# Optimization experiments

Measured on AMD Instinct MI355X. Metric: run time of the kernel, lower is better.

Reference implementation:

```python
import jax, jax.numpy as jnp
import numpy as np

N_NODES = 50000
N_EDGES = 800000
D_IN = 128
D_HID = 128
N_CLS = 47


def setup_inputs() -> dict:
    key = jax.random.key(0)
    ks = jax.random.split(key, 10)
    inp = {
        "features": jax.random.normal(ks[0], (N_NODES, D_IN), dtype=jnp.float32),
        "src": jax.random.randint(ks[1], (N_EDGES,), 0, N_NODES),
        "dst": jax.random.randint(ks[2], (N_EDGES,), 0, N_NODES),
        "Wself0": jax.random.normal(ks[3], (D_IN, D_HID), dtype=jnp.float32) / np.sqrt(D_IN),
        "Wneigh0": jax.random.normal(ks[4], (D_IN, D_HID), dtype=jnp.float32) / np.sqrt(D_IN),
        "b0": jnp.zeros((D_HID,), dtype=jnp.float32),
        "Wself1": jax.random.normal(ks[5], (D_HID, D_HID), dtype=jnp.float32) / np.sqrt(D_HID),
        "Wneigh1": jax.random.normal(ks[6], (D_HID, D_HID), dtype=jnp.float32) / np.sqrt(D_HID),
        "b1": jnp.zeros((D_HID,), dtype=jnp.float32),
        "Wself2": jax.random.normal(ks[7], (D_HID, N_CLS), dtype=jnp.float32) / np.sqrt(D_HID),
        "Wneigh2": jax.random.normal(ks[8], (D_HID, N_CLS), dtype=jnp.float32) / np.sqrt(D_HID),
        "b2": jnp.zeros((N_CLS,), dtype=jnp.float32),
    }
    return inp


def reference(features, src, dst, Wself0, Wneigh0, b0, Wself1, Wneigh1, b1, Wself2, Wneigh2, b2):
    # GraphSAGE (DGL SAGEConv, aggregator_type='mean', eval mode so dropout is identity).
    # Per layer: h_neigh[v] = mean_{(u->v) in E} h[u]; out = h @ W_self + h_neigh @ W_neigh + b
    n = features.shape[0]
    # in-degree for mean aggregation (zero-degree nodes get zero neighbor feature)
    deg = jax.ops.segment_sum(jnp.ones(dst.shape, dtype=features.dtype), dst, num_segments=n)
    inv_deg = (1.0 / jnp.maximum(deg, 1.0))[:, None]  # [N,1]

    def sage_layer(h, Ws, Wn, b, act):
        # gather src features per edge, scatter-add into dst, normalize by in-degree
        agg = jax.ops.segment_sum(h[src], dst, num_segments=n) * inv_deg  # [N, d]
        out = h @ Ws + agg @ Wn + b
        return jax.nn.relu(out) if act else out

    h = sage_layer(features, Wself0, Wneigh0, b0, True)
    h = sage_layer(h, Wself1, Wneigh1, b1, True)
    h = sage_layer(h, Wself2, Wneigh2, b2, False)
    return h
```

## Files before the change

kernel.cpp:

```cpp
#include <hip/hip_runtime.h>

#define D 128
#define NCLS 47
#define CAP 64

typedef short short8 __attribute__((ext_vector_type(8)));
typedef float floatx4 __attribute__((ext_vector_type(4)));
typedef unsigned short ushort8 __attribute__((ext_vector_type(8)));

__device__ inline float bf16lo(unsigned int u) {
    union { unsigned int i; float f; } c; c.i = u << 16; return c.f;
}
__device__ inline float bf16hi(unsigned int u) {
    union { unsigned int i; float f; } c; c.i = u & 0xffff0000u; return c.f;
}
__device__ inline unsigned short f2bf(float f) {
    union { float f; unsigned int i; } c; c.f = f;
    unsigned int r = c.i + 0x7fffu + ((c.i >> 16) & 1u);
    return (unsigned short)(r >> 16);
}
__device__ inline unsigned int pack2(float x, float y) {
    return (unsigned int)f2bf(x) | ((unsigned int)f2bf(y) << 16);
}

__global__ void zero_cnt_kernel(int* __restrict__ cnt, int n) {
    int i = blockIdx.x * blockDim.x + threadIdx.x;
    if (i < n) cnt[i] = 0;
}

#define FB 1024
#define PB 1024
__global__ __launch_bounds__(256) void fill_prep_kernel(
    const int* __restrict__ src, const int* __restrict__ dst,
    int* __restrict__ cnt, unsigned short* __restrict__ csr, int n_edges,
    const float* __restrict__ f, unsigned int* __restrict__ hA,
    unsigned int* __restrict__ hB, int npairs, int n,
    const float* __restrict__ Ws0, const float* __restrict__ Wn0, unsigned short* __restrict__ Wt0,
    const float* __restrict__ Ws1, const float* __restrict__ Wn1, unsigned short* __restrict__ Wt1,
    const float* __restrict__ Ws2, const float* __restrict__ Wn2, unsigned short* __restrict__ Wt2) {
    if (blockIdx.x < FB) {
        int cohort = blockIdx.x & 7;
        int cb = blockIdx.x >> 3;
        int nth = (FB >> 3) * 256;
        int tid = cb * 256 + threadIdx.x;
        int range = (n + 7) >> 3;
        int lo = cohort * range;
        int hi = lo + range;
        if (hi > n) hi = n;
        for (int e = tid; e < n_edges; e += nth) {
            int d = dst[e];
            if (d >= lo && d < hi) {
                int pos = atomicAdd(&cnt[d], 1);
                if (pos < CAP) csr[d * CAP + pos] = (unsigned short)src[e];
            }
        }
        return;
    }
    int tid = (blockIdx.x - FB) * 256 + threadIdx.x;
    int total = npairs + 128  + 2 * 128 * 256 + 48 * 256;
    for (int gid = tid; gid < total; gid += PB * 256) {
        if (gid < npairs) {
            float2 v = ((const float2*)f)[gid];
            hA[gid] = pack2(v.x, v.y);
            continue;
        }
        int r = gid - npairs;
        if (r < 128) {
            if (r < 64) hA[(size_t)n * 64 + r] = 0u;
            else hB[(size_t)n * 64 + (r - 64)] = 0u;
            continue;
        }
        r -= 128;
        if (r < 128 * 256) {
            int nn = r >> 8, k = r & 255;
            float v = (k < 128) ? Ws0[k * 128 + nn] : Wn0[(k - 128) * 128 + nn];
            Wt0[nn * 256 + k] = f2bf(v);
            continue;
        }
        r -= 128 * 256;
        if (r < 128 * 256) {
            int nn = r >> 8, k = r & 255;
            float v = (k < 128) ? Ws1[k * 128 + nn] : Wn1[(k - 128) * 128 + nn];
            Wt1[nn * 256 + k] = f2bf(v);
            continue;
        }
        r -= 128 * 256;
        if (r < 48 * 256) {
            int nn = r >> 8, k = r & 255;
            float v = 0.0f;
            if (nn < NCLS) v = (k < 128) ? Ws2[k * NCLS + nn] : Wn2[(k - 128) * NCLS + nn];
            Wt2[nn * 256 + k] = f2bf(v);
        }
    }
}

__global__ __launch_bounds__(256) void gather_kernel(
    const unsigned int* __restrict__ hin,
    const unsigned short* __restrict__ csr,
    const int* __restrict__ cnt,
    unsigned int* __restrict__ agg,
    int n) {
    int tid = blockIdx.x * blockDim.x + threadIdx.x;
    int node = tid >> 6;
    int lane = tid & 63;
    if (node >= n) return;
    int d = cnt[node];
    if (d > CAP) d = CAP;
    const unsigned short* crow = csr + node * CAP;
    float a0x = 0.f, a0y = 0.f, a1x = 0.f, a1y = 0.f;
    float a2x = 0.f, a2y = 0.f, a3x = 0.f, a3y = 0.f;
    int e = 0;
    for (; e + 8 <= d; e += 8) {
        ushort8 s = *(const ushort8*)(crow + e);
        unsigned int u0 = hin[(size_t)s[0] * 64 + lane];
        unsigned int u1 = hin[(size_t)s[1] * 64 + lane];
        unsigned int u2 = hin[(size_t)s[2] * 64 + lane];
        unsigned int u3 = hin[(size_t)s[3] * 64 + lane];
        unsigned int u4 = hin[(size_t)s[4] * 64 + lane];
        unsigned int u5 = hin[(size_t)s[5] * 64 + lane];
        unsigned int u6 = hin[(size_t)s[6] * 64 + lane];
        unsigned int u7 = hin[(size_t)s[7] * 64 + lane];
        a0x += bf16lo(u0); a0y += bf16hi(u0);
        a1x += bf16lo(u1); a1y += bf16hi(u1);
        a2x += bf16lo(u2); a2y += bf16hi(u2);
        a3x += bf16lo(u3); a3y += bf16hi(u3);
        a0x += bf16lo(u4); a0y += bf16hi(u4);
        a1x += bf16lo(u5); a1y += bf16hi(u5);
        a2x += bf16lo(u6); a2y += bf16hi(u6);
        a3x += bf16lo(u7); a3y += bf16hi(u7);
    }
    for (; e < d; ++e) {
        unsigned int u0 = hin[(size_t)crow[e] * 64 + lane];
        a0x += bf16lo(u0); a0y += bf16hi(u0);
    }
    float inv = 1.0f / fmaxf((float)d, 1.0f);
    float rx = ((a0x + a1x) + (a2x + a3x)) * inv;
    float ry = ((a0y + a1y) + (a2y + a3y)) * inv;
    agg[(size_t)node * 64 + lane] = pack2(rx, ry);
}

__global__ __launch_bounds__(256) void mfma_layer_kernel(
    const unsigned int* __restrict__ hin,
    const unsigned int* __restrict__ agg,
    const unsigned short* __restrict__ Wt,
    const float* __restrict__ bias,
    unsigned short* __restrict__ hout,
    int n) {
    int wave = threadIdx.x >> 6;
    int lane = threadIdx.x & 63;
    int node_base = blockIdx.x * 64 + wave * 16;
    int m = lane & 15;
    int quad = lane >> 4;
    int row_node = node_base + m;
    if (row_node >= n) row_node = n - 1;
    const unsigned short* arow = (const unsigned short*)hin + (size_t)row_node * 128;
    const unsigned short* grow = (const unsigned short*)agg + (size_t)row_node * 128;

    floatx4 acc[8];
#pragma unroll
    for (int t = 0; t < 8; ++t) acc[t] = (floatx4){0.f, 0.f, 0.f, 0.f};

#pragma unroll
    for (int ko = 0; ko < 128; ko += 32) {
        short8 a = *(const short8*)(arow + ko + quad * 8);
#pragma unroll
        for (int t = 0; t < 8; ++t) {
            short8 bfr = *(const short8*)(Wt + (size_t)(t * 16 + m) * 256 + ko + quad * 8);
            acc[t] = __builtin_amdgcn_mfma_f32_16x16x32_bf16(a, bfr, acc[t], 0, 0, 0);
        }
    }
#pragma unroll
    for (int ko = 0; ko < 128; ko += 32) {
        short8 a = *(const short8*)(grow + ko + quad * 8);
#pragma unroll
        for (int t = 0; t < 8; ++t) {
            short8 bfr = *(const short8*)(Wt + (size_t)(t * 16 + m) * 256 + 128 + ko + quad * 8);
            acc[t] = __builtin_amdgcn_mfma_f32_16x16x32_bf16(a, bfr, acc[t], 0, 0, 0);
        }
    }

#pragma unroll
    for (int t = 0; t < 8; ++t) {
        int nfeat = t * 16 + m;
        float bb = bias[nfeat];
#pragma unroll
        for (int r = 0; r < 4; ++r) {
            int node = node_base + quad * 4 + r;
            if (node < n) {
                float v = fmaxf(acc[t][r] + bb, 0.0f);
                hout[(size_t)node * 128 + nfeat] = f2bf(v);
            }
        }
    }
}

__global__ __launch_bounds__(256) void mfma_out_kernel(
    const unsigned int* __restrict__ hin,
    const unsigned int* __restrict__ agg,
    const unsigned short* __restrict__ Wt,
    const float* __restrict__ bias,
    float* __restrict__ out, int n) {
    int wave = threadIdx.x >> 6;
    int lane = threadIdx.x & 63;
    int node_base = blockIdx.x * 64 + wave * 16;
    int m = lane & 15;
    int quad = lane >> 4;
    int row_node = node_base + m;
    if (row_node >= n) row_node = n - 1;
    const unsigned short* arow = (const unsigned short*)hin + (size_t)row_node * 128;
    const unsigned short* grow = (const unsigned short*)agg + (size_t)row_node * 128;

    floatx4 acc[3];
#pragma unroll
    for (int t = 0; t < 3; ++t) acc[t] = (floatx4){0.f, 0.f, 0.f, 0.f};

#pragma unroll
    for (int ko = 0; ko < 128; ko += 32) {
        short8 a = *(const short8*)(arow + ko + quad * 8);
#pragma unroll
        for (int t = 0; t < 3; ++t) {
            short8 bfr = *(const short8*)(Wt + (size_t)(t * 16 + m) * 256 + ko + quad * 8);
            acc[t] = __builtin_amdgcn_mfma_f32_16x16x32_bf16(a, bfr, acc[t], 0, 0, 0);
        }
    }
#pragma unroll
    for (int ko = 0; ko < 128; ko += 32) {
        short8 a = *(const short8*)(grow + ko + quad * 8);
#pragma unroll
        for (int t = 0; t < 3; ++t) {
            short8 bfr = *(const short8*)(Wt + (size_t)(t * 16 + m) * 256 + 128 + ko + quad * 8);
            acc[t] = __builtin_amdgcn_mfma_f32_16x16x32_bf16(a, bfr, acc[t], 0, 0, 0);
        }
    }

#pragma unroll
    for (int t = 0; t < 3; ++t) {
        int nfeat = t * 16 + m;
        if (nfeat < NCLS) {
            float bb = bias[nfeat];
#pragma unroll
            for (int r = 0; r < 4; ++r) {
                int node = node_base + quad * 4 + r;
                if (node < n) out[(size_t)node * NCLS + nfeat] = acc[t][r] + bb;
            }
        }
    }
}

extern "C" void kernel_launch(void* const* d_in, const int* in_sizes, int n_in,
                              void* d_out, int out_size, void* d_ws, size_t ws_size,
                              hipStream_t stream) {
    const float* features = (const float*)d_in[0];
    const int* src = (const int*)d_in[1];
    const int* dst = (const int*)d_in[2];
    const float* Wself0 = (const float*)d_in[3];
    const float* Wneigh0 = (const float*)d_in[4];
    const float* b0 = (const float*)d_in[5];
    const float* Wself1 = (const float*)d_in[6];
    const float* Wneigh1 = (const float*)d_in[7];
    const float* b1 = (const float*)d_in[8];
    const float* Wself2 = (const float*)d_in[9];
    const float* Wneigh2 = (const float*)d_in[10];
    const float* b2 = (const float*)d_in[11];
    float* out = (float*)d_out;

    int n = in_sizes[0] / D;
    int n_edges = in_sizes[1];

    int* cnt = (int*)d_ws;
    unsigned short* csr = (unsigned short*)(cnt + 50048);
    unsigned int* hA = (unsigned int*)(csr + (size_t)n * CAP + 32);
    unsigned int* hB = hA + (size_t)(n + 1) * 64;
    unsigned int* agg = hB + (size_t)(n + 1) * 64;
    unsigned short* Wt0 = (unsigned short*)(agg + (size_t)n * 64);
    unsigned short* Wt1 = Wt0 + 128 * 256;
    unsigned short* Wt2 = Wt1 + 128 * 256;

    int npairs = n * 64;

    zero_cnt_kernel<<<(n + 255) / 256, 256, 0, stream>>>(cnt, n);
    fill_prep_kernel<<<FB + PB, 256, 0, stream>>>(
        src, dst, cnt, csr, n_edges,
        features, hA, hB, npairs, n,
        Wself0, Wneigh0, Wt0, Wself1, Wneigh1, Wt1, Wself2, Wneigh2, Wt2);

    int gather_blocks = (n * 64 + 255) / 256;
    int gemm_blocks = (n + 63) / 64;

    gather_kernel<<<gather_blocks, 256, 0, stream>>>(hA, csr, cnt, agg, n);
    mfma_layer_kernel<<<gemm_blocks, 256, 0, stream>>>(hA, agg, Wt0, b0, (unsigned short*)hB, n);
    gather_kernel<<<gather_blocks, 256, 0, stream>>>(hB, csr, cnt, agg, n);
    mfma_layer_kernel<<<gemm_blocks, 256, 0, stream>>>(hB, agg, Wt1, b1, (unsigned short*)hA, n);
    gather_kernel<<<gather_blocks, 256, 0, stream>>>(hA, csr, cnt, agg, n);
    mfma_out_kernel<<<gemm_blocks, 256, 0, stream>>>(hA, agg, Wt2, b2, out, n);
}
```

Measured before the change: 344.9 us.

## Fuse all stages into one persistent cooperative kernel with grid syncs

Replaces the eight separate launches (zero, fill/prep, three gathers, three GEMMs) with a single cooperative persistent kernel that separates the phases with grid-wide barriers, and keeps the multi-launch path as a fallback. Each stage becomes a grid-stride loop over nodes or tiles. The aim is to remove per-launch overhead and the idle tail between launches. In exchange the grid is capped at a fixed size, so gather and GEMM get fewer concurrent waves than the oversubscribed launches had, and each grid sync has its own cost. The zeroing of the padding rows of hA/hB is dropped, which looks harmless because the gather never reads index n.

After: 359.8 us. 1.04x slower.

```diff
diff --git a/kernel.cpp b/kernel.cpp
--- a/kernel.cpp
+++ b/kernel.cpp
@@ -1,4 +1,7 @@
 #include <hip/hip_runtime.h>
+#include <hip/hip_cooperative_groups.h>
+
+namespace cg = cooperative_groups;
 
 #define D 128
 #define NCLS 47
@@ -8,69 +11,64 @@
 typedef float floatx4 __attribute__((ext_vector_type(4)));
 typedef unsigned short ushort8 __attribute__((ext_vector_type(8)));
 
-__device__ inline float bf16lo(unsigned int u) {
+__device__ __forceinline__ float bf16lo(unsigned int u) {
     union { unsigned int i; float f; } c; c.i = u << 16; return c.f;
 }
-__device__ inline float bf16hi(unsigned int u) {
+__device__ __forceinline__ float bf16hi(unsigned int u) {
     union { unsigned int i; float f; } c; c.i = u & 0xffff0000u; return c.f;
 }
-__device__ inline unsigned short f2bf(float f) {
+__device__ __forceinline__ unsigned short f2bf(float f) {
     union { float f; unsigned int i; } c; c.f = f;
     unsigned int r = c.i + 0x7fffu + ((c.i >> 16) & 1u);
     return (unsigned short)(r >> 16);
 }
-__device__ inline unsigned int pack2(float x, float y) {
+__device__ __forceinline__ unsigned int pack2(float x, float y) {
     return (unsigned int)f2bf(x) | ((unsigned int)f2bf(y) << 16);
 }
 
-__global__ void zero_cnt_kernel(int* __restrict__ cnt, int n) {
-    int i = blockIdx.x * blockDim.x + threadIdx.x;
-    if (i < n) cnt[i] = 0;
-}
-
-#define FB 1024
-#define PB 1024
-__global__ __launch_bounds__(256) void fill_prep_kernel(
-    const int* __restrict__ src, const int* __restrict__ dst,
-    int* __restrict__ cnt, unsigned short* __restrict__ csr, int n_edges,
-    const float* __restrict__ f, unsigned int* __restrict__ hA,
-    unsigned int* __restrict__ hB, int npairs, int n,
+
+__device__ __forceinline__ void dev_zero(int* __restrict__ cnt, int n) {
+    int tid = blockIdx.x * blockDim.x + threadIdx.x;
+    int stride = gridDim.x * blockDim.x;
+    for (int i = tid; i < n; i += stride) cnt[i] = 0;
+}
+
+__device__ __forceinline__ void dev_fill(const int* __restrict__ src, const int* __restrict__ dst,
+                                         int* __restrict__ cnt, unsigned short* __restrict__ csr,
+                                         int n_edges, int n, int FBm) {
+    int cohort = blockIdx.x & 7;
+    int cb = blockIdx.x >> 3;
+    int nth = (FBm >> 3) * 256;
+    int tid = cb * 256 + threadIdx.x;
+    int range = (n + 7) >> 3;
+    int lo = cohort * range;
+    int hi = lo + range;
+    if (hi > n) hi = n;
+    for (int e = tid; e < n_edges; e += nth) {
+        int d = dst[e];
+        if (d >= lo && d < hi) {
+            int pos = atomicAdd(&cnt[d], 1);
+            if (pos < CAP) csr[d * CAP + pos] = (unsigned short)src[e];
+        }
+    }
+}
+
+__device__ __forceinline__ void dev_prep(
+    const float* __restrict__ f, unsigned int* __restrict__ hA, int npairs,
     const float* __restrict__ Ws0, const float* __restrict__ Wn0, unsigned short* __restrict__ Wt0,
     const float* __restrict__ Ws1, const float* __restrict__ Wn1, unsigned short* __restrict__ Wt1,
-    const float* __restrict__ Ws2, const float* __restrict__ Wn2, unsigned short* __restrict__ Wt2) {
-    if (blockIdx.x < FB) {
-        int cohort = blockIdx.x & 7;
-        int cb = blockIdx.x >> 3;
-        int nth = (FB >> 3) * 256;
-        int tid = cb * 256 + threadIdx.x;
-        int range = (n + 7) >> 3;
-        int lo = cohort * range;
-        int hi = lo + range;
-        if (hi > n) hi = n;
-        for (int e = tid; e < n_edges; e += nth) {
-            int d = dst[e];
-            if (d >= lo && d < hi) {
-                int pos = atomicAdd(&cnt[d], 1);
-                if (pos < CAP) csr[d * CAP + pos] = (unsigned short)src[e];
-            }
-        }
-        return;
-    }
-    int tid = (blockIdx.x - FB) * 256 + threadIdx.x;
-    int total = npairs + 128  + 2 * 128 * 256 + 48 * 256;
-    for (int gid = tid; gid < total; gid += PB * 256) {
+    const float* __restrict__ Ws2, const float* __restrict__ Wn2, unsigned short* __restrict__ Wt2,
+    int FBm) {
+    int tid = (blockIdx.x - FBm) * 256 + threadIdx.x;
+    int stride = (gridDim.x - FBm) * 256;
+    int total = npairs + 2 * 128 * 256 + 48 * 256;
+    for (int gid = tid; gid < total; gid += stride) {
         if (gid < npairs) {
             float2 v = ((const float2*)f)[gid];
             hA[gid] = pack2(v.x, v.y);
             continue;
         }
         int r = gid - npairs;
-        if (r < 128) {
-            if (r < 64) hA[(size_t)n * 64 + r] = 0u;
-            else hB[(size_t)n * 64 + (r - 64)] = 0u;
-            continue;
-        }
-        r -= 128;
         if (r < 128 * 256) {
             int nn = r >> 8, k = r & 255;
             float v = (k < 128) ? Ws0[k * 128 + nn] : Wn0[(k - 128) * 128 + nn];
@@ -94,157 +92,232 @@
     }
 }
 
-__global__ __launch_bounds__(256) void gather_kernel(
-    const unsigned int* __restrict__ hin,
-    const unsigned short* __restrict__ csr,
-    const int* __restrict__ cnt,
-    unsigned int* __restrict__ agg,
-    int n) {
-    int tid = blockIdx.x * blockDim.x + threadIdx.x;
-    int node = tid >> 6;
-    int lane = tid & 63;
-    if (node >= n) return;
-    int d = cnt[node];
-    if (d > CAP) d = CAP;
-    const unsigned short* crow = csr + node * CAP;
-    float a0x = 0.f, a0y = 0.f, a1x = 0.f, a1y = 0.f;
-    float a2x = 0.f, a2y = 0.f, a3x = 0.f, a3y = 0.f;
-    int e = 0;
-    for (; e + 8 <= d; e += 8) {
-        ushort8 s = *(const ushort8*)(crow + e);
-        unsigned int u0 = hin[(size_t)s[0] * 64 + lane];
-        unsigned int u1 = hin[(size_t)s[1] * 64 + lane];
-        unsigned int u2 = hin[(size_t)s[2] * 64 + lane];
-        unsigned int u3 = hin[(size_t)s[3] * 64 + lane];
-        unsigned int u4 = hin[(size_t)s[4] * 64 + lane];
-        unsigned int u5 = hin[(size_t)s[5] * 64 + lane];
-        unsigned int u6 = hin[(size_t)s[6] * 64 + lane];
-        unsigned int u7 = hin[(size_t)s[7] * 64 + lane];
-        a0x += bf16lo(u0); a0y += bf16hi(u0);
-        a1x += bf16lo(u1); a1y += bf16hi(u1);
-        a2x += bf16lo(u2); a2y += bf16hi(u2);
-        a3x += bf16lo(u3); a3y += bf16hi(u3);
-        a0x += bf16lo(u4); a0y += bf16hi(u4);
-        a1x += bf16lo(u5); a1y += bf16hi(u5);
-        a2x += bf16lo(u6); a2y += bf16hi(u6);
-        a3x += bf16lo(u7); a3y += bf16hi(u7);
-    }
-    for (; e < d; ++e) {
-        unsigned int u0 = hin[(size_t)crow[e] * 64 + lane];
-        a0x += bf16lo(u0); a0y += bf16hi(u0);
-    }
-    float inv = 1.0f / fmaxf((float)d, 1.0f);
-    float rx = ((a0x + a1x) + (a2x + a3x)) * inv;
-    float ry = ((a0y + a1y) + (a2y + a3y)) * inv;
-    agg[(size_t)node * 64 + lane] = pack2(rx, ry);
-}
-
-__global__ __launch_bounds__(256) void mfma_layer_kernel(
-    const unsigned int* __restrict__ hin,
-    const unsigned int* __restrict__ agg,
-    const unsigned short* __restrict__ Wt,
-    const float* __restrict__ bias,
-    unsigned short* __restrict__ hout,
-    int n) {
+__device__ __forceinline__ void dev_gather(const unsigned int* __restrict__ hin,
+                                           const unsigned short* __restrict__ csr,
+                                           const int* __restrict__ cnt,
+                                           unsigned int* __restrict__ agg, int n) {
+    int gw = (blockIdx.x * blockDim.x + threadIdx.x) >> 6;
+    int lane = threadIdx.x & 63;
+    int nwaves = (gridDim.x * blockDim.x) >> 6;
+    for (int node = gw; node < n; node += nwaves) {
+        int d = cnt[node];
+        if (d > CAP) d = CAP;
+        const unsigned short* crow = csr + node * CAP;
+        float a0x = 0.f, a0y = 0.f, a1x = 0.f, a1y = 0.f;
+        float a2x = 0.f, a2y = 0.f, a3x = 0.f, a3y = 0.f;
+        int e = 0;
+        for (; e + 8 <= d; e += 8) {
+            ushort8 s = *(const ushort8*)(crow + e);
+            unsigned int u0 = hin[(size_t)s[0] * 64 + lane];
+            unsigned int u1 = hin[(size_t)s[1] * 64 + lane];
+            unsigned int u2 = hin[(size_t)s[2] * 64 + lane];
+            unsigned int u3 = hin[(size_t)s[3] * 64 + lane];
+            unsigned int u4 = hin[(size_t)s[4] * 64 + lane];
+            unsigned int u5 = hin[(size_t)s[5] * 64 + lane];
+            unsigned int u6 = hin[(size_t)s[6] * 64 + lane];
+            unsigned int u7 = hin[(size_t)s[7] * 64 + lane];
+            a0x += bf16lo(u0); a0y += bf16hi(u0);
+            a1x += bf16lo(u1); a1y += bf16hi(u1);
+            a2x += bf16lo(u2); a2y += bf16hi(u2);
+            a3x += bf16lo(u3); a3y += bf16hi(u3);
+            a0x += bf16lo(u4); a0y += bf16hi(u4);
+            a1x += bf16lo(u5); a1y += bf16hi(u5);
+            a2x += bf16lo(u6); a2y += bf16hi(u6);
+            a3x += bf16lo(u7); a3y += bf16hi(u7);
+        }
+        for (; e < d; ++e) {
+            unsigned int u0 = hin[(size_t)crow[e] * 64 + lane];
+            a0x += bf16lo(u0); a0y += bf16hi(u0);
+        }
+        float inv = 1.0f / fmaxf((float)d, 1.0f);
+        float rx = ((a0x + a1x) + (a2x + a3x)) * inv;
+        float ry = ((a0y + a1y) + (a2y + a3y)) * inv;
+        agg[(size_t)node * 64 + lane] = pack2(rx, ry);
+    }
+}
+
+__device__ __forceinline__ void dev_mfma(const unsigned int* __restrict__ hin,
+                                         const unsigned int* __restrict__ agg,
+                                         const unsigned short* __restrict__ Wt,
+                                         const float* __restrict__ bias,
+                                         unsigned short* __restrict__ hout, int n) {
     int wave = threadIdx.x >> 6;
     int lane = threadIdx.x & 63;
-    int node_base = blockIdx.x * 64 + wave * 16;
     int m = lane & 15;
     int quad = lane >> 4;
-    int row_node = node_base + m;
-    if (row_node >= n) row_node = n - 1;
-    const unsigned short* arow = (const unsigned short*)hin + (size_t)row_node * 128;
-    const unsigned short* grow = (const unsigned short*)agg + (size_t)row_node * 128;
-
-    floatx4 acc[8];
-#pragma unroll
-    for (int t = 0; t < 8; ++t) acc[t] = (floatx4){0.f, 0.f, 0.f, 0.f};
-
-#pragma unroll
-    for (int ko = 0; ko < 128; ko += 32) {
-        short8 a = *(const short8*)(arow + ko + quad * 8);
+    int ntiles = (n + 63) >> 6;
+    for (int tile = blockIdx.x; tile < ntiles; tile += gridDim.x) {
+        int node_base = tile * 64 + wave * 16;
+        int row_node = node_base + m;
+        if (row_node >= n) row_node = n - 1;
+        const unsigned short* arow = (const unsigned short*)hin + (size_t)row_node * 128;
+        const unsigned short* grow = (const unsigned short*)agg + (size_t)row_node * 128;
+
+        floatx4 acc[8];
+#pragma unroll
+        for (int t = 0; t < 8; ++t) acc[t] = (floatx4){0.f, 0.f, 0.f, 0.f};
+#pragma unroll
+        for (int ko = 0; ko < 128; ko += 32) {
+            short8 a = *(const short8*)(arow + ko + quad * 8);
+#pragma unroll
+            for (int t = 0; t < 8; ++t) {
+                short8 bfr = *(const short8*)(Wt + (size_t)(t * 16 + m) * 256 + ko + quad * 8);
+                acc[t] = __builtin_amdgcn_mfma_f32_16x16x32_bf16(a, bfr, acc[t], 0, 0, 0);
+            }
+        }
+#pragma unroll
+        for (int ko = 0; ko < 128; ko += 32) {
+            short8 a = *(const short8*)(grow + ko + quad * 8);
+#pragma unroll
+            for (int t = 0; t < 8; ++t) {
+                short8 bfr = *(const short8*)(Wt + (size_t)(t * 16 + m) * 256 + 128 + ko + quad * 8);
+                acc[t] = __builtin_amdgcn_mfma_f32_16x16x32_bf16(a, bfr, acc[t], 0, 0, 0);
+            }
+        }
 #pragma unroll
         for (int t = 0; t < 8; ++t) {
-            short8 bfr = *(const short8*)(Wt + (size_t)(t * 16 + m) * 256 + ko + quad * 8);
-            acc[t] = __builtin_amdgcn_mfma_f32_16x16x32_bf16(a, bfr, acc[t], 0, 0, 0);
-        }
-    }
-#pragma unroll
-    for (int ko = 0; ko < 128; ko += 32) {
-        short8 a = *(const short8*)(grow + ko + quad * 8);
-#pragma unroll
-        for (int t = 0; t < 8; ++t) {
-            short8 bfr = *(const short8*)(Wt + (size_t)(t * 16 + m) * 256 + 128 + ko + quad * 8);
-            acc[t] = __builtin_amdgcn_mfma_f32_16x16x32_bf16(a, bfr, acc[t], 0, 0, 0);
-        }
-    }
-
-#pragma unroll
-    for (int t = 0; t < 8; ++t) {
-        int nfeat = t * 16 + m;
-        float bb = bias[nfeat];
-#pragma unroll
-        for (int r = 0; r < 4; ++r) {
-            int node = node_base + quad * 4 + r;
-            if (node < n) {
-                float v = fmaxf(acc[t][r] + bb, 0.0f);
-                hout[(size_t)node * 128 + nfeat] = f2bf(v);
-            }
-        }
-    }
-}
-
-__global__ __launch_bounds__(256) void mfma_out_kernel(
-    const unsigned int* __restrict__ hin,
-    const unsigned int* __restrict__ agg,
-    const unsigned short* __restrict__ Wt,
-    const float* __restrict__ bias,
-    float* __restrict__ out, int n) {
+            int nfeat = t * 16 + m;
+            float bb = bias[nfeat];
+#pragma unroll
+            for (int r = 0; r < 4; ++r) {
+                int node = node_base + quad * 4 + r;
+                if (node < n) {
+                    float v = fmaxf(acc[t][r] + bb, 0.0f);
+                    hout[(size_t)node * 128 + nfeat] = f2bf(v);
+                }
+            }
+        }
+    }
+}
+
+__device__ __forceinline__ void dev_mfma_out(const unsigned int* __restrict__ hin,
+                                             const unsigned int* __restrict__ agg,
+                                             const unsigned short* __restrict__ Wt,
+                                             const float* __restrict__ bias,
+                                             float* __restrict__ out, int n) {
     int wave = threadIdx.x >> 6;
     int lane = threadIdx.x & 63;
-    int node_base = blockIdx.x * 64 + wave * 16;
     int m = lane & 15;
     int quad = lane >> 4;
-    int row_node = node_base + m;
-    if (row_node >= n) row_node = n - 1;
-    const unsigned short* arow = (const unsigned short*)hin + (size_t)row_node * 128;
-    const unsigned short* grow = (const unsigned short*)agg + (size_t)row_node * 128;
-
-    floatx4 acc[3];
-#pragma unroll
-    for (int t = 0; t < 3; ++t) acc[t] = (floatx4){0.f, 0.f, 0.f, 0.f};
-
-#pragma unroll
-    for (int ko = 0; ko < 128; ko += 32) {
-        short8 a = *(const short8*)(arow + ko + quad * 8);
+    int ntiles = (n + 63) >> 6;
+    for (int tile = blockIdx.x; tile < ntiles; tile += gridDim.x) {
+        int node_base = tile * 64 + wave * 16;
+        int row_node = node_base + m;
+        if (row_node >= n) row_node = n - 1;
+        const unsigned short* arow = (const unsigned short*)hin + (size_t)row_node * 128;
+        const unsigned short* grow = (const unsigned short*)agg + (size_t)row_node * 128;
+
+        floatx4 acc[3];
+#pragma unroll
+        for (int t = 0; t < 3; ++t) acc[t] = (floatx4){0.f, 0.f, 0.f, 0.f};
+#pragma unroll
+        for (int ko = 0; ko < 128; ko += 32) {
+            short8 a = *(const short8*)(arow + ko + quad * 8);
+#pragma unroll
+            for (int t = 0; t < 3; ++t) {
+                short8 bfr = *(const short8*)(Wt + (size_t)(t * 16 + m) * 256 + ko + quad * 8);
+                acc[t] = __builtin_amdgcn_mfma_f32_16x16x32_bf16(a, bfr, acc[t], 0, 0, 0);
+            }
+        }
+#pragma unroll
+        for (int ko = 0; ko < 128; ko += 32) {
+            short8 a = *(const short8*)(grow + ko + quad * 8);
+#pragma unroll
+            for (int t = 0; t < 3; ++t) {
+                short8 bfr = *(const short8*)(Wt + (size_t)(t * 16 + m) * 256 + 128 + ko + quad * 8);
+                acc[t] = __builtin_amdgcn_mfma_f32_16x16x32_bf16(a, bfr, acc[t], 0, 0, 0);
+            }
+        }
 #pragma unroll
         for (int t = 0; t < 3; ++t) {
-            short8 bfr = *(const short8*)(Wt + (size_t)(t * 16 + m) * 256 + ko + quad * 8);
-            acc[t] = __builtin_amdgcn_mfma_f32_16x16x32_bf16(a, bfr, acc[t], 0, 0, 0);
-        }
-    }
-#pragma unroll
-    for (int ko = 0; ko < 128; ko += 32) {
-        short8 a = *(const short8*)(grow + ko + quad * 8);
-#pragma unroll
-        for (int t = 0; t < 3; ++t) {
-            short8 bfr = *(const short8*)(Wt + (size_t)(t * 16 + m) * 256 + 128 + ko + quad * 8);
-            acc[t] = __builtin_amdgcn_mfma_f32_16x16x32_bf16(a, bfr, acc[t], 0, 0, 0);
-        }
-    }
-
-#pragma unroll
-    for (int t = 0; t < 3; ++t) {
-        int nfeat = t * 16 + m;
-        if (nfeat < NCLS) {
-            float bb = bias[nfeat];
-#pragma unroll
-            for (int r = 0; r < 4; ++r) {
-                int node = node_base + quad * 4 + r;
-                if (node < n) out[(size_t)node * NCLS + nfeat] = acc[t][r] + bb;
-            }
-        }
-    }
+            int nfeat = t * 16 + m;
+            if (nfeat < NCLS) {
+                float bb = bias[nfeat];
+#pragma unroll
+                for (int r = 0; r < 4; ++r) {
+                    int node = node_base + quad * 4 + r;
+                    if (node < n) out[(size_t)node * NCLS + nfeat] = acc[t][r] + bb;
+                }
+            }
+        }
+    }
+}
+
+
+__global__ __launch_bounds__(256) void mega_kernel(
+    const float* f, const int* src, const int* dst,
+    const float* Ws0, const float* Wn0, const float* b0,
+    const float* Ws1, const float* Wn1, const float* b1,
+    const float* Ws2, const float* Wn2, const float* b2,
+    float* out,
+    int* cnt, unsigned short* csr, unsigned int* hA, unsigned int* hB, unsigned int* agg,
+    unsigned short* Wt0, unsigned short* Wt1, unsigned short* Wt2,
+    int n, int n_edges) {
+    cg::grid_group g = cg::this_grid();
+
+    dev_zero(cnt, n);
+    g.sync();
+
+    int G = gridDim.x;
+    int FBm = (G * 2 / 3) & ~7;
+    if (FBm < 8) FBm = 8;
+    if (FBm >= G) FBm = G - 8;
+    int npairs = n * 64;
+    if ((int)blockIdx.x < FBm)
+        dev_fill(src, dst, cnt, csr, n_edges, n, FBm);
+    else
+        dev_prep(f, hA, npairs, Ws0, Wn0, Wt0, Ws1, Wn1, Wt1, Ws2, Wn2, Wt2, FBm);
+    g.sync();
+
+    dev_gather(hA, csr, cnt, agg, n);
+    g.sync();
+    dev_mfma(hA, agg, Wt0, b0, (unsigned short*)hB, n);
+    g.sync();
+    dev_gather(hB, csr, cnt, agg, n);
+    g.sync();
+    dev_mfma(hB, agg, Wt1, b1, (unsigned short*)hA, n);
+    g.sync();
+    dev_gather(hA, csr, cnt, agg, n);
+    g.sync();
+    dev_mfma_out(hA, agg, Wt2, b2, out, n);
+}
+
+
+__global__ void zero_cnt_kernel(int* cnt, int n) { dev_zero(cnt, n); }
+
+__global__ __launch_bounds__(256) void fill_prep_kernel(
+    const int* src, const int* dst, int* cnt, unsigned short* csr, int n_edges,
+    const float* f, unsigned int* hA, int npairs, int n,
+    const float* Ws0, const float* Wn0, unsigned short* Wt0,
+    const float* Ws1, const float* Wn1, unsigned short* Wt1,
+    const float* Ws2, const float* Wn2, unsigned short* Wt2) {
+    const int FBm = 1024;
+    if ((int)blockIdx.x < FBm)
+        dev_fill(src, dst, cnt, csr, n_edges, n, FBm);
+    else
+        dev_prep(f, hA, npairs, Ws0, Wn0, Wt0, Ws1, Wn1, Wt1, Ws2, Wn2, Wt2, FBm);
+}
+
+__global__ __launch_bounds__(256) void gather_kernel(const unsigned int* hin,
+                                                     const unsigned short* csr,
+                                                     const int* cnt, unsigned int* agg, int n) {
+    dev_gather(hin, csr, cnt, agg, n);
+}
+
+__global__ __launch_bounds__(256) void mfma_layer_kernel(const unsigned int* hin,
+                                                         const unsigned int* agg,
+                                                         const unsigned short* Wt,
+                                                         const float* bias,
+                                                         unsigned short* hout, int n) {
+    dev_mfma(hin, agg, Wt, bias, hout, n);
+}
+
+__global__ __launch_bounds__(256) void mfma_out_kernel(const unsigned int* hin,
+                                                       const unsigned int* agg,
+                                                       const unsigned short* Wt,
+                                                       const float* bias,
+                                                       float* out, int n) {
+    dev_mfma_out(hin, agg, Wt, bias, out, n);
 }
 
 extern "C" void kernel_launch(void* const* d_in, const int* in_sizes, int n_in,
@@ -253,14 +326,14 @@
     const float* features = (const float*)d_in[0];
     const int* src = (const int*)d_in[1];
     const int* dst = (const int*)d_in[2];
-    const float* Wself0 = (const float*)d_in[3];
-    const float* Wneigh0 = (const float*)d_in[4];
+    const float* Ws0 = (const float*)d_in[3];
+    const float* Wn0 = (const float*)d_in[4];
     const float* b0 = (const float*)d_in[5];
-    const float* Wself1 = (const float*)d_in[6];
-    const float* Wneigh1 = (const float*)d_in[7];
+    const float* Ws1 = (const float*)d_in[6];
+    const float* Wn1 = (const float*)d_in[7];
     const float* b1 = (const float*)d_in[8];
-    const float* Wself2 = (const float*)d_in[9];
-    const float* Wneigh2 = (const float*)d_in[10];
+    const float* Ws2 = (const float*)d_in[9];
+    const float* Wn2 = (const float*)d_in[10];
     const float* b2 = (const float*)d_in[11];
     float* out = (float*)d_out;
 
@@ -276,21 +349,42 @@
     unsigned short* Wt1 = Wt0 + 128 * 256;
     unsigned short* Wt2 = Wt1 + 128 * 256;
 
-    int npairs = n * 64;
-
-    zero_cnt_kernel<<<(n + 255) / 256, 256, 0, stream>>>(cnt, n);
-    fill_prep_kernel<<<FB + PB, 256, 0, stream>>>(
-        src, dst, cnt, csr, n_edges,
-        features, hA, hB, npairs, n,
-        Wself0, Wneigh0, Wt0, Wself1, Wneigh1, Wt1, Wself2, Wneigh2, Wt2);
-
-    int gather_blocks = (n * 64 + 255) / 256;
-    int gemm_blocks = (n + 63) / 64;
-
-    gather_kernel<<<gather_blocks, 256, 0, stream>>>(hA, csr, cnt, agg, n);
-    mfma_layer_kernel<<<gemm_blocks, 256, 0, stream>>>(hA, agg, Wt0, b0, (unsigned short*)hB, n);
-    gather_kernel<<<gather_blocks, 256, 0, stream>>>(hB, csr, cnt, agg, n);
-    mfma_layer_kernel<<<gemm_blocks, 256, 0, stream>>>(hB, agg, Wt1, b1, (unsigned short*)hA, n);
-    gather_kernel<<<gather_blocks, 256, 0, stream>>>(hA, csr, cnt, agg, n);
-    mfma_out_kernel<<<gemm_blocks, 256, 0, stream>>>(hA, agg, Wt2, b2, out, n);
-}
+    int nb = 0;
+    hipError_t oerr = hipOccupancyMaxActiveBlocksPerMultiprocessor(
+        &nb, (const void*)mega_kernel, 256, 0);
+    bool coop_ok = false;
+    if (oerr == hipSuccess && nb >= 1) {
+        int G = nb * 256;
+        if (G > 2048) G = 2048;
+        if (G >= 24) {
+            void* kargs[] = {
+                (void*)&features, (void*)&src, (void*)&dst,
+                (void*)&Ws0, (void*)&Wn0, (void*)&b0,
+                (void*)&Ws1, (void*)&Wn1, (void*)&b1,
+                (void*)&Ws2, (void*)&Wn2, (void*)&b2,
+                (void*)&out,
+                (void*)&cnt, (void*)&csr, (void*)&hA, (void*)&hB, (void*)&agg,
+                (void*)&Wt0, (void*)&Wt1, (void*)&Wt2,
+                (void*)&n, (void*)&n_edges};
+            hipError_t lerr = hipLaunchCooperativeKernel(
+                (const void*)mega_kernel, dim3(G), dim3(256), kargs, 0, stream);
+            coop_ok = (lerr == hipSuccess);
+        }
+    }
+
+    if (!coop_ok) {
+        int npairs = n * 64;
+        zero_cnt_kernel<<<(n + 255) / 256, 256, 0, stream>>>(cnt, n);
+        fill_prep_kernel<<<2048, 256, 0, stream>>>(
+            src, dst, cnt, csr, n_edges, features, hA, npairs, n,
+            Ws0, Wn0, Wt0, Ws1, Wn1, Wt1, Ws2, Wn2, Wt2);
+        int gather_blocks = (n * 64 + 255) / 256;
+        int gemm_blocks = (n + 63) / 64;
+        gather_kernel<<<gather_blocks, 256, 0, stream>>>(hA, csr, cnt, agg, n);
+        mfma_layer_kernel<<<gemm_blocks, 256, 0, stream>>>(hA, agg, Wt0, b0, (unsigned short*)hB, n);
+        gather_kernel<<<gather_blocks, 256, 0, stream>>>(hB, csr, cnt, agg, n);
+        mfma_layer_kernel<<<gemm_blocks, 256, 0, stream>>>(hB, agg, Wt1, b1, (unsigned short*)hA, n);
+        gather_kernel<<<gather_blocks, 256, 0, stream>>>(hA, csr, cnt, agg, n);
+        mfma_out_kernel<<<gemm_blocks, 256, 0, stream>>>(hA, agg, Wt2, b2, out, n);
+    }
+}
```
